# Kernel optimization log

Hardware: AMD Instinct MI355X
Metric: run time of the kernel (lower is better)

Reference implementation:

```python
import jax, jax.numpy as jnp
import numpy as np
import math

B, A, IN_C, OUT_C = 64, 128, 128, 64

def _l2norm(x, eps=1e-12):
    # matches F.normalize(dim=1) on 2D input: x / max(||x||_2, eps) along last dim
    n = jnp.sqrt(jnp.sum(x * x, axis=-1, keepdims=True))
    return x / jnp.maximum(n, eps)

def setup_inputs() -> dict:
    key = jax.random.key(0)
    ks = jax.random.split(key, 7)
    s = 1.0 / math.sqrt(IN_C)
    return {
        "features": jax.random.normal(ks[0], (B, IN_C, A), dtype=jnp.float32),
        "Wq": jax.random.uniform(ks[1], (OUT_C, IN_C), jnp.float32, -s, s),
        "bq": jax.random.uniform(ks[2], (OUT_C,), jnp.float32, -s, s),
        "Wk": jax.random.uniform(ks[3], (OUT_C, IN_C), jnp.float32, -s, s),
        "bk": jax.random.uniform(ks[4], (OUT_C,), jnp.float32, -s, s),
        "Wv": jax.random.uniform(ks[5], (OUT_C, IN_C), jnp.float32, -s, s),
        "bv": jax.random.uniform(ks[6], (OUT_C,), jnp.float32, -s, s),
    }

def reference(features, Wq, bq, Wk, bk, Wv, bv):
    b = features.shape[0]
    f = jnp.transpose(features, (0, 2, 1))          # (b, a, in_c)
    a = f.shape[1]
    q = f @ Wq.T + bq                               # (b, a, d)
    k = f @ Wk.T + bk
    v = f @ Wv.T + bv
    d = q.shape[-1]
    qf = q.reshape(-1, d)                           # (N, d), N = b*a
    kf = k.reshape(-1, d)
    vf = v.reshape(-1, d)
    att = jax.nn.softmax(qf @ kf.T / math.sqrt(d), axis=1)  # (N, N)
    qkv = att @ vf                                  # (N, d)
    qkv_n = _l2norm(qkv).reshape(b, a, d)
    v_n = _l2norm(vf).reshape(b, a, d)
    # sim_s[i,j] = (1/a) * sum_t v_n[i,t] . qkv_n[j,t]  (diagonal-trace over 'a')
    sim_s = jnp.einsum('bad,cad->bc', v_n, qkv_n) / a
    return sim_s
```

## Files before the change

### kernel.cpp

```cpp
#include <hip/hip_runtime.h>
#include <hip/hip_bf16.h>

#define NROW 8192
#define INC  128
#define OUTC 64
#define BG   16

#define QSCALE 0.18033688011112042f

typedef __bf16 bf16x8 __attribute__((ext_vector_type(8)));
typedef __bf16 bf16x4 __attribute__((ext_vector_type(4)));
typedef short  s16x4  __attribute__((ext_vector_type(4)));
typedef short  s16x8  __attribute__((ext_vector_type(8)));
typedef float  f32x4  __attribute__((ext_vector_type(4)));

static __device__ __forceinline__ f32x4 mfma16(bf16x8 a, bf16x8 b, f32x4 c) {
    return __builtin_amdgcn_mfma_f32_16x16x32_bf16(a, b, c, 0, 0, 0);
}
static __device__ __forceinline__ f32x4 mfma1k(s16x4 a, s16x4 b, f32x4 c) {
    return __builtin_amdgcn_mfma_f32_16x16x16bf16_1k(a, b, c, 0, 0, 0);
}

static __device__ __forceinline__ bf16x8 cvt8(float4 lo, float4 hi) {
    bf16x8 r;
    r[0] = (__bf16)lo.x; r[1] = (__bf16)lo.y; r[2] = (__bf16)lo.z; r[3] = (__bf16)lo.w;
    r[4] = (__bf16)hi.x; r[5] = (__bf16)hi.y; r[6] = (__bf16)hi.z; r[7] = (__bf16)hi.w;
    return r;
}
static __device__ __forceinline__ s16x4 vlo(s16x8 x) {
    return __builtin_shufflevector(x, x, 0, 1, 2, 3);
}
static __device__ __forceinline__ s16x4 vhi(s16x8 x) {
    return __builtin_shufflevector(x, x, 4, 5, 6, 7);
}

__global__ __launch_bounds__(256) void proj_kernel(
    const float* __restrict__ feat,
    const float* __restrict__ Wq, const float* __restrict__ bq,
    const float* __restrict__ Wk, const float* __restrict__ bk,
    const float* __restrict__ Wv, const float* __restrict__ bv,
    __hip_bfloat16* __restrict__ qbf, __hip_bfloat16* __restrict__ kbf,
    __hip_bfloat16* __restrict__ vbf, __hip_bfloat16* __restrict__ vnb)
{
    __shared__ float slab[32 * 132];
    __shared__ float vbuf[32 * 66];
    __shared__ float invb[32];

    const int blk = blockIdx.x;
    const int b   = blk >> 2;
    const int a0  = (blk & 3) * 32;
    const int r0  = b * 128 + a0;
    const float* fb = feat + (size_t)b * INC * 128;

    for (int i = threadIdx.x; i < 32 * 128; i += 256) {
        int c = i >> 5, a = i & 31;
        slab[a * 132 + c] = fb[c * 128 + a0 + a];
    }
    __syncthreads();

    const int w    = threadIdx.x >> 6;
    const int lane = threadIdx.x & 63;
    const int l16  = lane & 15;
    const int quad = lane >> 4;

    f32x4 acc[3][2];
    #pragma unroll
    for (int t = 0; t < 3; ++t)
        #pragma unroll
        for (int u = 0; u < 2; ++u)
            acc[t][u] = (f32x4){0.f, 0.f, 0.f, 0.f};

    #pragma unroll
    for (int kc = 0; kc < 4; ++kc) {
        const int k0 = kc * 32 + quad * 8;
        bf16x8 afr[2];
        #pragma unroll
        for (int u = 0; u < 2; ++u) {
            const float* ar = slab + (u * 16 + l16) * 132 + k0;
            afr[u] = cvt8(*(const float4*)ar, *(const float4*)(ar + 4));
        }
        #pragma unroll
        for (int t = 0; t < 3; ++t) {
            const int tile = w * 3 + t;
            const int mat  = tile >> 2;
            const float* W = (mat == 0) ? Wq : (mat == 1) ? Wk : Wv;
            const float* wr = W + ((tile & 3) * 16 + l16) * INC + k0;
            bf16x8 bfr = cvt8(*(const float4*)wr, *(const float4*)(wr + 4));
            #pragma unroll
            for (int u = 0; u < 2; ++u)
                acc[t][u] = mfma16(afr[u], bfr, acc[t][u]);
        }
    }

    #pragma unroll
    for (int t = 0; t < 3; ++t) {
        const int tile = w * 3 + t;
        const int mat  = tile >> 2;
        const int nt   = tile & 3;
        const float* bias = (mat == 0) ? bq : (mat == 1) ? bk : bv;
        const float bl = bias[nt * 16 + l16];
        if (mat < 2) {
            const float sc = (mat == 0) ? QSCALE : 1.0f;
            __hip_bfloat16* dst = mat ? kbf : qbf;
            #pragma unroll
            for (int u = 0; u < 2; ++u) {
                const int base = ((((r0 >> 4) + u) * 4 + nt) << 8) + l16;
                #pragma unroll
                for (int r = 0; r < 4; ++r)
                    dst[base + (quad * 4 + r) * 16] = __float2bfloat16((acc[t][u][r] + bl) * sc);
            }
        } else {
            #pragma unroll
            for (int u = 0; u < 2; ++u)
                #pragma unroll
                for (int r = 0; r < 4; ++r)
                    vbuf[(u * 16 + quad * 4 + r) * 66 + nt * 16 + l16] = acc[t][u][r] + bl;
        }
    }
    __syncthreads();

    const int rl = threadIdx.x >> 3;
    const int jj = threadIdx.x & 7;
    float ss = 0.f;
    #pragma unroll
    for (int i = 0; i < 8; ++i) {
        float x = vbuf[rl * 66 + jj * 8 + i];
        ss += x * x;
    }
    ss += __shfl_xor(ss, 1, 64);
    ss += __shfl_xor(ss, 2, 64);
    ss += __shfl_xor(ss, 4, 64);
    if (jj == 0) invb[rl] = rsqrtf(fmaxf(ss, 1e-24f));
    __syncthreads();
    float inv = invb[rl];
    bf16x8 vp;
    #pragma unroll
    for (int i = 0; i < 8; ++i)
        vp[i] = (__bf16)(vbuf[rl * 66 + jj * 8 + i] * inv);
    *(bf16x8*)(vnb + (size_t)(r0 + rl) * 64 + jj * 8) = vp;

    const int tl = threadIdx.x & 15;
    const int n  = (threadIdx.x >> 4) & 3;
    const int s_ = threadIdx.x >> 6;
    bf16x8 pack;
    #pragma unroll
    for (int j = 0; j < 8; ++j) {
        int key = s_ * 8 + j;
        pack[j] = (__bf16)(vbuf[key * 66 + n * 16 + tl] * invb[key]);
    }
    const int hblk = (r0 >> 4) + (s_ >> 1);
    const int eb = hblk * 1024 + (n >> 1) * 512 + tl * 32 + (s_ & 1) * 16 + (n & 1) * 4;
    bf16x4 plo = __builtin_shufflevector(pack, pack, 0, 1, 2, 3);
    bf16x4 phi = __builtin_shufflevector(pack, pack, 4, 5, 6, 7);
    *(bf16x4*)(vbf + eb)     = plo;
    *(bf16x4*)(vbf + eb + 8) = phi;
}

#define ATTN_ITER(K00,K01,K10,K11, NK00,NK01,NK10,NK11,                      \
                  W0,W1,W2,W3, NW0,NW1,NW2,NW3)                              \
    do {                                                                     \
        NW0 = *(const s16x8*)(vp);                            \
        NW1 = *(const s16x8*)(vp + 1024);                     \
        NW2 = *(const s16x8*)(vp + 2048);                     \
        NW3 = *(const s16x8*)(vp + 3072);                     \
        NK00 = *(const bf16x8*)(kp);                                         \
        NK01 = *(const bf16x8*)(kp + 1024);                                  \
        NK10 = *(const bf16x8*)(kp + 2048);                                  \
        NK11 = *(const bf16x8*)(kp + 3072);                                  \
        vp += 4096; kp += 4096;                                              \
        const f32x4 zero = (f32x4){0.f, 0.f, 0.f, 0.f};                      \
        _Pragma("unroll")                                                    \
        for (int u = 0; u < 4; ++u) {                                        \
            f32x4 s0 = mfma16(K00, qf32[u][0], zero);                        \
            s0       = mfma16(K01, qf32[u][1], s0);                          \
            f32x4 s1 = mfma16(K10, qf32[u][0], zero);                        \
            s1       = mfma16(K11, qf32[u][1], s1);                          \
            union { bf16x4 v; s16x4 s; } pf0, pf1;                           \
            _Pragma("unroll")                                                \
            for (int r = 0; r < 4; ++r) {                                    \
                float p0 = __builtin_amdgcn_exp2f(s0[r]);                    \
                float p1 = __builtin_amdgcn_exp2f(s1[r]);                    \
                lp[u] += p0 + p1;                                            \
                pf0.v[r] = (__bf16)p0;                                       \
                pf1.v[r] = (__bf16)p1;                                       \
            }                                                                \
            of[u][0] = mfma1k(pf0.s, vlo(W0), of[u][0]);                     \
            of[u][0] = mfma1k(pf1.s, vlo(W2), of[u][0]);                     \
            of[u][1] = mfma1k(pf0.s, vhi(W0), of[u][1]);                     \
            of[u][1] = mfma1k(pf1.s, vhi(W2), of[u][1]);                     \
            of[u][2] = mfma1k(pf0.s, vlo(W1), of[u][2]);                     \
            of[u][2] = mfma1k(pf1.s, vlo(W3), of[u][2]);                     \
            of[u][3] = mfma1k(pf0.s, vhi(W1), of[u][3]);                     \
            of[u][3] = mfma1k(pf1.s, vhi(W3), of[u][3]);                     \
        }                                                                    \
    } while (0)

__global__ __launch_bounds__(256, 2) void attn_kernel(
    const __hip_bfloat16* __restrict__ qbf,
    const __hip_bfloat16* __restrict__ kbf,
    const __hip_bfloat16* __restrict__ vbf,
    float* __restrict__ Opart, float* __restrict__ lpart)
{
    const int qb    = blockIdx.x >> 4;
    const int bg    = blockIdx.x & 15;
    const int w     = threadIdx.x >> 6;
    const int lane  = threadIdx.x & 63;
    const int l16   = lane & 15;
    const int quad  = lane >> 4;
    const int r0    = qb * 256 + w * 64;
    const int fo32  = l16 * 16 + (quad & 1) * 8;
    const int qh    = quad >> 1;

    bf16x8 qf32[4][2];
    #pragma unroll
    for (int u = 0; u < 4; ++u)
        #pragma unroll
        for (int p = 0; p < 2; ++p)
            qf32[u][p] = *(const bf16x8*)(qbf +
                ((((r0 >> 4) + u) * 4 + p * 2 + qh) << 8) + fo32);

    f32x4 of[4][4];
    float lp[4] = {0.f, 0.f, 0.f, 0.f};
    #pragma unroll
    for (int u = 0; u < 4; ++u)
        #pragma unroll
        for (int n = 0; n < 4; ++n)
            of[u][n] = (f32x4){0.f, 0.f, 0.f, 0.f};

    const int ck0 = bg * 32;
    const char* kp = (const char*)kbf + ck0 * 2048 + qh * 512 + fo32 * 2;
    const char* vp = (const char*)vbf + ck0 * 2048 + l16 * 64 + quad * 16;

    bf16x8 kA00, kA01, kA10, kA11, kB00, kB01, kB10, kB11;
    s16x8  wA0, wA1, wA2, wA3, wB0, wB1, wB2, wB3;

    wA0 = *(const s16x8*)(vp);
    wA1 = *(const s16x8*)(vp + 1024);
    wA2 = *(const s16x8*)(vp + 2048);
    wA3 = *(const s16x8*)(vp + 3072);
    kA00 = *(const bf16x8*)(kp);
    kA01 = *(const bf16x8*)(kp + 1024);
    kA10 = *(const bf16x8*)(kp + 2048);
    kA11 = *(const bf16x8*)(kp + 3072);
    vp += 4096; kp += 4096;

    #pragma unroll 1
    for (int body = 0; body < 8; ++body) {
        ATTN_ITER(kA00, kA01, kA10, kA11, kB00, kB01, kB10, kB11,
                  wA0, wA1, wA2, wA3, wB0, wB1, wB2, wB3);
        ATTN_ITER(kB00, kB01, kB10, kB11, kA00, kA01, kA10, kA11,
                  wB0, wB1, wB2, wB3, wA0, wA1, wA2, wA3);
    }

    #pragma unroll
    for (int u = 0; u < 4; ++u) {
        float v = lp[u];
        v += __shfl_xor(v, 16, 64);
        v += __shfl_xor(v, 32, 64);
        lp[u] = v;
    }

    const int task = (qb * 4 + w) * 16 + bg;
    float* Ob = Opart + (size_t)task * 4096;
    #pragma unroll
    for (int u = 0; u < 4; ++u)
        #pragma unroll
        for (int n = 0; n < 4; ++n)
            #pragma unroll
            for (int r = 0; r < 4; ++r)
                Ob[(u * 16 + quad * 4 + r) * 64 + n * 16 + l16] = of[u][n][r];
    if (quad == 0) {
        #pragma unroll
        for (int u = 0; u < 4; ++u)
            lpart[task * 64 + u * 16 + l16] = lp[u];
    }
}

__global__ __launch_bounds__(256) void combine_kernel(
    const float* __restrict__ Opart, const float* __restrict__ lpart,
    __hip_bfloat16* __restrict__ qnb, float* __restrict__ outz)
{
    if (blockIdx.x == 0) {
        #pragma unroll
        for (int z = 0; z < 4; ++z)
            ((float4*)outz)[threadIdx.x * 4 + z] = (float4){0.f, 0.f, 0.f, 0.f};
    }

    const int r    = blockIdx.x * 4 + (threadIdx.x >> 6);
    const int c    = threadIdx.x & 63;
    const int tile = r >> 6, row = r & 63;
    float acc = 0.f, lsum = 0.f;
    #pragma unroll
    for (int g = 0; g < 16; ++g) {
        int task = tile * 16 + g;
        acc  += Opart[(size_t)task * 4096 + row * 64 + c];
        lsum += lpart[task * 64 + row];
    }
    float q = acc / lsum;
    float ss = q * q;
    ss += __shfl_xor(ss, 1, 64);
    ss += __shfl_xor(ss, 2, 64);
    ss += __shfl_xor(ss, 4, 64);
    ss += __shfl_xor(ss, 8, 64);
    ss += __shfl_xor(ss, 16, 64);
    ss += __shfl_xor(ss, 32, 64);
    qnb[(size_t)r * 64 + c] = __float2bfloat16(q * rsqrtf(fmaxf(ss, 1e-24f)));
}

__global__ __launch_bounds__(256) void sim_kernel(
    const __hip_bfloat16* __restrict__ vnb,
    const __hip_bfloat16* __restrict__ qnb,
    float* __restrict__ out)
{
    const int w    = threadIdx.x >> 6;
    const int lane = threadIdx.x & 63;
    const int l16  = lane & 15;
    const int quad = lane >> 4;
    const int k0   = blockIdx.x * 128 + w * 32 + quad * 8;

    f32x4 acc[4][4];
    #pragma unroll
    for (int mi = 0; mi < 4; ++mi)
        #pragma unroll
        for (int ni = 0; ni < 4; ++ni)
            acc[mi][ni] = (f32x4){0.f, 0.f, 0.f, 0.f};

    bf16x8 af[4], bfv[4];
    #pragma unroll
    for (int mi = 0; mi < 4; ++mi)
        af[mi] = *(const bf16x8*)(vnb + (size_t)(mi * 16 + l16) * 8192 + k0);
    #pragma unroll
    for (int ni = 0; ni < 4; ++ni)
        bfv[ni] = *(const bf16x8*)(qnb + (size_t)(ni * 16 + l16) * 8192 + k0);
    #pragma unroll
    for (int mi = 0; mi < 4; ++mi)
        #pragma unroll
        for (int ni = 0; ni < 4; ++ni)
            acc[mi][ni] = mfma16(af[mi], bfv[ni], acc[mi][ni]);

    #pragma unroll
    for (int mi = 0; mi < 4; ++mi)
        #pragma unroll
        for (int ni = 0; ni < 4; ++ni)
            #pragma unroll
            for (int r = 0; r < 4; ++r)
                atomicAdd(&out[(mi * 16 + quad * 4 + r) * 64 + ni * 16 + l16],
                          acc[mi][ni][r] * (1.f / 128.f));
}

extern "C" void kernel_launch(void* const* d_in, const int* in_sizes, int n_in,
                              void* d_out, int out_size, void* d_ws, size_t ws_size,
                              hipStream_t stream)
{
    const float* feat = (const float*)d_in[0];
    const float* Wq   = (const float*)d_in[1];
    const float* bq   = (const float*)d_in[2];
    const float* Wk   = (const float*)d_in[3];
    const float* bk   = (const float*)d_in[4];
    const float* Wv   = (const float*)d_in[5];
    const float* bv   = (const float*)d_in[6];
    float* out = (float*)d_out;

    const size_t MB = 1u << 20;
    char* ws = (char*)d_ws;
    __hip_bfloat16* qbf = (__hip_bfloat16*)(ws);
    __hip_bfloat16* kbf = (__hip_bfloat16*)(ws + 1 * MB);
    __hip_bfloat16* vbf = (__hip_bfloat16*)(ws + 2 * MB);
    __hip_bfloat16* vnb = (__hip_bfloat16*)(ws + 3 * MB);
    float* Opart = (float*)(ws + 4 * MB);
    float* lpart = (float*)(ws + 36 * MB);
    __hip_bfloat16* qnb = (__hip_bfloat16*)(ws + 37 * MB);

    proj_kernel<<<256, 256, 0, stream>>>(feat, Wq, bq, Wk, bk, Wv, bv, qbf, kbf, vbf, vnb);
    attn_kernel<<<512, 256, 0, stream>>>(qbf, kbf, vbf, Opart, lpart);
    combine_kernel<<<2048, 256, 0, stream>>>(Opart, lpart, qnb, out);
    sim_kernel<<<64, 256, 0, stream>>>(vnb, qnb, out);
}
```

Measured before the change: 123.1 us.

## Stage K/V tiles through double-buffered LDS shared across waves in attention

Changes the global layout of the K and V bf16 buffers so that each 4 KB chunk matches the per-lane fragment order. The attention kernel now has the whole block cooperatively load each chunk once into a double-buffered LDS tile, and every wave then reads its fragments from LDS. Before, each of the four waves loaded the same K/V data from global memory into its own registers. This cuts redundant global/L2 traffic and register pressure, but adds LDS round trips and a __syncthreads per chunk.

```diff
diff --git a/kernel.cpp b/kernel.cpp
--- a/kernel.cpp
+++ b/kernel.cpp
@@ -99,16 +99,23 @@
         const int nt   = tile & 3;
         const float* bias = (mat == 0) ? bq : (mat == 1) ? bk : bv;
         const float bl = bias[nt * 16 + l16];
-        if (mat < 2) {
-            const float sc = (mat == 0) ? QSCALE : 1.0f;
-            __hip_bfloat16* dst = mat ? kbf : qbf;
+        if (mat == 0) {
             #pragma unroll
             for (int u = 0; u < 2; ++u) {
                 const int base = ((((r0 >> 4) + u) * 4 + nt) << 8) + l16;
                 #pragma unroll
                 for (int r = 0; r < 4; ++r)
-                    dst[base + (quad * 4 + r) * 16] = __float2bfloat16((acc[t][u][r] + bl) * sc);
+                    qbf[base + (quad * 4 + r) * 16] =
+                        __float2bfloat16((acc[t][u][r] + bl) * QSCALE);
             }
+        } else if (mat == 1) {
+            const int kq = (r0 >> 5) * 2048 + (nt >> 1) * 512 +
+                           ((nt & 1) * 2 + (l16 >> 3)) * 128 + quad * 32 + (l16 & 7);
+            #pragma unroll
+            for (int u = 0; u < 2; ++u)
+                #pragma unroll
+                for (int r = 0; r < 4; ++r)
+                    kbf[kq + u * 1024 + r * 8] = __float2bfloat16(acc[t][u][r] + bl);
         } else {
             #pragma unroll
             for (int u = 0; u < 2; ++u)
@@ -148,52 +155,57 @@
         int key = s_ * 8 + j;
         pack[j] = (__bf16)(vbuf[key * 66 + n * 16 + tl] * invb[key]);
     }
-    const int hblk = (r0 >> 4) + (s_ >> 1);
-    const int eb = hblk * 1024 + (n >> 1) * 512 + tl * 32 + (s_ & 1) * 16 + (n & 1) * 4;
+    const int e1 = (r0 >> 5) * 2048 + (s_ >> 1) * 1024 + (n >> 1) * 512 +
+                   (s_ & 1) * 256 + tl * 8 + (n & 1) * 4;
     bf16x4 plo = __builtin_shufflevector(pack, pack, 0, 1, 2, 3);
     bf16x4 phi = __builtin_shufflevector(pack, pack, 4, 5, 6, 7);
-    *(bf16x4*)(vbf + eb)     = plo;
-    *(bf16x4*)(vbf + eb + 8) = phi;
-}
-
-#define ATTN_ITER(K00,K01,K10,K11, NK00,NK01,NK10,NK11,                      \
-                  W0,W1,W2,W3, NW0,NW1,NW2,NW3)                              \
-    do {                                                                     \
-        NW0 = *(const s16x8*)(vp);                            \
-        NW1 = *(const s16x8*)(vp + 1024);                     \
-        NW2 = *(const s16x8*)(vp + 2048);                     \
-        NW3 = *(const s16x8*)(vp + 3072);                     \
-        NK00 = *(const bf16x8*)(kp);                                         \
-        NK01 = *(const bf16x8*)(kp + 1024);                                  \
-        NK10 = *(const bf16x8*)(kp + 2048);                                  \
-        NK11 = *(const bf16x8*)(kp + 3072);                                  \
-        vp += 4096; kp += 4096;                                              \
-        const f32x4 zero = (f32x4){0.f, 0.f, 0.f, 0.f};                      \
+    *(bf16x4*)(vbf + e1)       = plo;
+    *(bf16x4*)(vbf + e1 + 128) = phi;
+}
+
+#define STAGE_W(BUF, KR, VR) do {                                            \
+        *(float4*)((BUF) + stb) = KR;                                        \
+        *(float4*)((BUF) + 4096 + stb) = VR; } while (0)
+#define STAGE_L(KR, VR) do {                                                 \
+        KR = *(const float4*)gk; VR = *(const float4*)gv;                    \
+        gk += 4096; gv += 4096; } while (0)
+
+#define COMPUTE(BUF) do {                                                    \
+    const char* kbp = (BUF);                                                 \
+    const char* vbp = (BUF) + 4096;                                          \
+    bf16x8 k00 = *(const bf16x8*)(kbp + lb);                                 \
+    bf16x8 k01 = *(const bf16x8*)(kbp + lb + 1024);                          \
+    bf16x8 k10 = *(const bf16x8*)(kbp + lb + 2048);                          \
+    bf16x8 k11 = *(const bf16x8*)(kbp + lb + 3072);                          \
+    s16x8 W0 = *(const s16x8*)(vbp + lb);                                    \
+    s16x8 W1 = *(const s16x8*)(vbp + lb + 1024);                             \
+    s16x8 W2 = *(const s16x8*)(vbp + lb + 2048);                             \
+    s16x8 W3 = *(const s16x8*)(vbp + lb + 3072);                             \
+    const f32x4 zero = (f32x4){0.f, 0.f, 0.f, 0.f};                          \
+    _Pragma("unroll")                                                        \
+    for (int u = 0; u < 4; ++u) {                                            \
+        f32x4 s0 = mfma16(k00, qf32[u][0], zero);                            \
+        s0       = mfma16(k01, qf32[u][1], s0);                              \
+        f32x4 s1 = mfma16(k10, qf32[u][0], zero);                            \
+        s1       = mfma16(k11, qf32[u][1], s1);                              \
+        union { bf16x4 v; s16x4 s; } pf0, pf1;                               \
         _Pragma("unroll")                                                    \
-        for (int u = 0; u < 4; ++u) {                                        \
-            f32x4 s0 = mfma16(K00, qf32[u][0], zero);                        \
-            s0       = mfma16(K01, qf32[u][1], s0);                          \
-            f32x4 s1 = mfma16(K10, qf32[u][0], zero);                        \
-            s1       = mfma16(K11, qf32[u][1], s1);                          \
-            union { bf16x4 v; s16x4 s; } pf0, pf1;                           \
-            _Pragma("unroll")                                                \
-            for (int r = 0; r < 4; ++r) {                                    \
-                float p0 = __builtin_amdgcn_exp2f(s0[r]);                    \
-                float p1 = __builtin_amdgcn_exp2f(s1[r]);                    \
-                lp[u] += p0 + p1;                                            \
-                pf0.v[r] = (__bf16)p0;                                       \
-                pf1.v[r] = (__bf16)p1;                                       \
-            }                                                                \
-            of[u][0] = mfma1k(pf0.s, vlo(W0), of[u][0]);                     \
-            of[u][0] = mfma1k(pf1.s, vlo(W2), of[u][0]);                     \
-            of[u][1] = mfma1k(pf0.s, vhi(W0), of[u][1]);                     \
-            of[u][1] = mfma1k(pf1.s, vhi(W2), of[u][1]);                     \
-            of[u][2] = mfma1k(pf0.s, vlo(W1), of[u][2]);                     \
-            of[u][2] = mfma1k(pf1.s, vlo(W3), of[u][2]);                     \
-            of[u][3] = mfma1k(pf0.s, vhi(W1), of[u][3]);                     \
-            of[u][3] = mfma1k(pf1.s, vhi(W3), of[u][3]);                     \
+        for (int r = 0; r < 4; ++r) {                                        \
+            float p0 = __builtin_amdgcn_exp2f(s0[r]);                        \
+            float p1 = __builtin_amdgcn_exp2f(s1[r]);                        \
+            lp[u] += p0 + p1;                                                \
+            pf0.v[r] = (__bf16)p0;                                           \
+            pf1.v[r] = (__bf16)p1;                                           \
         }                                                                    \
-    } while (0)
+        of[u][0] = mfma1k(pf0.s, vlo(W0), of[u][0]);                         \
+        of[u][0] = mfma1k(pf1.s, vlo(W2), of[u][0]);                         \
+        of[u][1] = mfma1k(pf0.s, vhi(W0), of[u][1]);                         \
+        of[u][1] = mfma1k(pf1.s, vhi(W2), of[u][1]);                         \
+        of[u][2] = mfma1k(pf0.s, vlo(W1), of[u][2]);                         \
+        of[u][2] = mfma1k(pf1.s, vlo(W3), of[u][2]);                         \
+        of[u][3] = mfma1k(pf0.s, vhi(W1), of[u][3]);                         \
+        of[u][3] = mfma1k(pf1.s, vhi(W3), of[u][3]);                         \
+    } } while (0)
 
 __global__ __launch_bounds__(256, 2) void attn_kernel(
     const __hip_bfloat16* __restrict__ qbf,
@@ -201,15 +213,22 @@
     const __hip_bfloat16* __restrict__ vbf,
     float* __restrict__ Opart, float* __restrict__ lpart)
 {
+    __shared__ float4 ldsq[2][512];
+    char* bufA = (char*)&ldsq[0][0];
+    char* bufB = (char*)&ldsq[1][0];
+
     const int qb    = blockIdx.x >> 4;
     const int bg    = blockIdx.x & 15;
-    const int w     = threadIdx.x >> 6;
-    const int lane  = threadIdx.x & 63;
+    const int tid   = threadIdx.x;
+    const int w     = tid >> 6;
+    const int lane  = tid & 63;
     const int l16   = lane & 15;
     const int quad  = lane >> 4;
     const int r0    = qb * 256 + w * 64;
     const int fo32  = l16 * 16 + (quad & 1) * 8;
     const int qh    = quad >> 1;
+    const int lb    = lane * 16;
+    const int stb   = tid * 16;
 
     bf16x8 qf32[4][2];
     #pragma unroll
@@ -227,30 +246,30 @@
         for (int n = 0; n < 4; ++n)
             of[u][n] = (f32x4){0.f, 0.f, 0.f, 0.f};
 
-    const int ck0 = bg * 32;
-    const char* kp = (const char*)kbf + ck0 * 2048 + qh * 512 + fo32 * 2;
-    const char* vp = (const char*)vbf + ck0 * 2048 + l16 * 64 + quad * 16;
-
-    bf16x8 kA00, kA01, kA10, kA11, kB00, kB01, kB10, kB11;
-    s16x8  wA0, wA1, wA2, wA3, wB0, wB1, wB2, wB3;
-
-    wA0 = *(const s16x8*)(vp);
-    wA1 = *(const s16x8*)(vp + 1024);
-    wA2 = *(const s16x8*)(vp + 2048);
-    wA3 = *(const s16x8*)(vp + 3072);
-    kA00 = *(const bf16x8*)(kp);
-    kA01 = *(const bf16x8*)(kp + 1024);
-    kA10 = *(const bf16x8*)(kp + 2048);
-    kA11 = *(const bf16x8*)(kp + 3072);
-    vp += 4096; kp += 4096;
+    const char* gk = (const char*)kbf + (size_t)(bg * 16) * 4096 + stb;
+    const char* gv = (const char*)vbf + (size_t)(bg * 16) * 4096 + stb;
+
+    float4 ka, va, kb_, vb_;
+    STAGE_L(ka, va);
+    STAGE_W(bufA, ka, va);
+    STAGE_L(kb_, vb_);
+    __syncthreads();
 
     #pragma unroll 1
-    for (int body = 0; body < 8; ++body) {
-        ATTN_ITER(kA00, kA01, kA10, kA11, kB00, kB01, kB10, kB11,
-                  wA0, wA1, wA2, wA3, wB0, wB1, wB2, wB3);
-        ATTN_ITER(kB00, kB01, kB10, kB11, kA00, kA01, kA10, kA11,
-                  wB0, wB1, wB2, wB3, wA0, wA1, wA2, wA3);
-    }
+    for (int body = 0; body < 7; ++body) {
+        STAGE_W(bufB, kb_, vb_);
+        STAGE_L(ka, va);
+        COMPUTE(bufA);
+        __syncthreads();
+        STAGE_W(bufA, ka, va);
+        STAGE_L(kb_, vb_);
+        COMPUTE(bufB);
+        __syncthreads();
+    }
+    STAGE_W(bufB, kb_, vb_);
+    COMPUTE(bufA);
+    __syncthreads();
+    COMPUTE(bufB);
 
     #pragma unroll
     for (int u = 0; u < 4; ++u) {
```

Measured after the change: 121.6 us. About the same (-1.2%).
